# Kernel optimization log

Measured on AMD Instinct MI355X. Metric: run time of the kernel, lower is better.

Reference implementation:

```python
import jax, jax.numpy as jnp
import numpy as np

N, E, NIN, NOUT, H = 50000, 800000, 128, 128, 8
C = NOUT // H  # head dim = 16


def setup_inputs() -> dict:
    key = jax.random.key(0)
    ks = jax.random.split(key, 12)
    s = 1.0 / np.sqrt(NIN)
    return {
        "x": jax.random.normal(ks[0], (N, NIN), dtype=jnp.float32),
        "edge_index": jax.random.randint(ks[1], (2, E), 0, N),
        "edge_attr": jax.random.normal(ks[2], (E, NIN), dtype=jnp.float32),
        "Wq": jax.random.normal(ks[3], (NIN, H * C), dtype=jnp.float32) * s,
        "bq": jnp.zeros((H * C,), dtype=jnp.float32),
        "Wk": jax.random.normal(ks[4], (NIN, H * C), dtype=jnp.float32) * s,
        "bk": jnp.zeros((H * C,), dtype=jnp.float32),
        "Wv": jax.random.normal(ks[5], (NIN, H * C), dtype=jnp.float32) * s,
        "bv": jnp.zeros((H * C,), dtype=jnp.float32),
        "We": jax.random.normal(ks[6], (NIN, H * C), dtype=jnp.float32) * s,  # lin_edge, bias=False in PyG
        "Wskip": jax.random.normal(ks[7], (NIN, H * C), dtype=jnp.float32) * s,
        "bskip": jnp.zeros((H * C,), dtype=jnp.float32),
    }


def reference(x, edge_index, edge_attr, Wq, bq, Wk, bk, Wv, bv, We, Wskip, bskip):
    src = edge_index[0]  # j (source / message sender)
    dst = edge_index[1]  # i (destination / aggregation target)

    q = (x @ Wq + bq).reshape(N, H, C)
    k = (x @ Wk + bk).reshape(N, H, C)
    v = (x @ Wv + bv).reshape(N, H, C)
    e = (edge_attr @ We).reshape(E, H, C)

    k_e = k[src] + e                                   # [E,H,C]
    alpha = jnp.einsum('ehc,ehc->eh', q[dst], k_e) / jnp.sqrt(jnp.float32(C))

    # segment softmax over incoming edges of each destination node
    m = jax.ops.segment_max(alpha, dst, num_segments=N)            # [N,H]
    a = jnp.exp(alpha - m[dst])                                    # [E,H]
    z = jax.ops.segment_sum(a, dst, num_segments=N)                # [N,H]
    a = a / (z[dst] + 1e-16)

    msg = (v[src] + e) * a[:, :, None]                             # [E,H,C]
    out = jax.ops.segment_sum(msg, dst, num_segments=N)            # [N,H,C]
    out = out.reshape(N, H * C) + (x @ Wskip + bskip)              # root skip
    return out
```

## Files before the change

### kernel.cpp

```cpp
#include <hip/hip_runtime.h>


#define N_NODES 50000
#define N_EDGES 800000
#define DIN     128
#define DHC     128
#define NHEAD   8
#define HDIM    16
#define BK      32
#define LDAT    132

static_assert(N_EDGES % 128 == 0, "edge tiles exact");

__global__ __launch_bounds__(256) void node_gemm_kernel(
    const float* __restrict__ x,
    const float* __restrict__ Wq, const float* __restrict__ bq,
    const float* __restrict__ Wk, const float* __restrict__ bk,
    const float* __restrict__ Wv, const float* __restrict__ bv,
    const float* __restrict__ Wskip, const float* __restrict__ bskip,
    float* __restrict__ Q, float* __restrict__ K,
    float* __restrict__ V, float* __restrict__ SKIP)
{
    __shared__ float sXT[BK * LDAT];
    __shared__ float sW[BK * LDAT];

    const float* W; const float* bias; float* OUT;
    switch (blockIdx.y) {
        case 0:  W = Wq;    bias = bq;    OUT = Q;    break;
        case 1:  W = Wk;    bias = bk;    OUT = K;    break;
        case 2:  W = Wv;    bias = bv;    OUT = V;    break;
        default: W = Wskip; bias = bskip; OUT = SKIP; break;
    }

    const int tid  = threadIdx.x;
    const int row0 = blockIdx.x * 128;
    const int r0   = (tid >> 4) * 4;
    const int c0   = (tid & 15) * 4;

    float acc[8][8];
    #pragma unroll
    for (int i = 0; i < 8; ++i)
        #pragma unroll
        for (int j = 0; j < 8; ++j) acc[i][j] = 0.f;

    for (int kk = 0; kk < DIN; kk += BK) {
        #pragma unroll
        for (int p = 0; p < 4; ++p) {
            int i = tid + p * 256;
            int k = i >> 5, c4 = i & 31;
            ((float4*)&sW[k * LDAT])[c4] =
                ((const float4*)(W + (size_t)(kk + k) * DHC))[c4];
        }
        #pragma unroll
        for (int p = 0; p < 4; ++p) {
            int el = (tid >> 3) + p * 32;
            int c4 = tid & 7;
            int r  = row0 + el;
            float4 v = (r < N_NODES)
                ? ((const float4*)(x + (size_t)r * DIN + kk))[c4]
                : make_float4(0.f, 0.f, 0.f, 0.f);
            int kl = c4 * 4;
            sXT[(kl + 0) * LDAT + el] = v.x;
            sXT[(kl + 1) * LDAT + el] = v.y;
            sXT[(kl + 2) * LDAT + el] = v.z;
            sXT[(kl + 3) * LDAT + el] = v.w;
        }
        __syncthreads();

        #pragma unroll 4
        for (int k = 0; k < BK; ++k) {
            float4 a0 = *(const float4*)&sXT[k * LDAT + r0];
            float4 a1 = *(const float4*)&sXT[k * LDAT + r0 + 64];
            float4 b0 = *(const float4*)&sW[k * LDAT + c0];
            float4 b1 = *(const float4*)&sW[k * LDAT + c0 + 64];
            float a[8] = {a0.x, a0.y, a0.z, a0.w, a1.x, a1.y, a1.z, a1.w};
            float b[8] = {b0.x, b0.y, b0.z, b0.w, b1.x, b1.y, b1.z, b1.w};
            #pragma unroll
            for (int i = 0; i < 8; ++i)
                #pragma unroll
                for (int j = 0; j < 8; ++j)
                    acc[i][j] = fmaf(a[i], b[j], acc[i][j]);
        }
        __syncthreads();
    }

    float bcol[8];
    #pragma unroll
    for (int j = 0; j < 8; ++j) bcol[j] = bias[c0 + ((j < 4) ? j : j + 60)];

    #pragma unroll
    for (int i = 0; i < 8; ++i) {
        int r = row0 + r0 + ((i < 4) ? i : i + 60);
        if (r < N_NODES) {
            float4 o0 = make_float4(acc[i][0] + bcol[0], acc[i][1] + bcol[1],
                                    acc[i][2] + bcol[2], acc[i][3] + bcol[3]);
            float4 o1 = make_float4(acc[i][4] + bcol[4], acc[i][5] + bcol[5],
                                    acc[i][6] + bcol[6], acc[i][7] + bcol[7]);
            *(float4*)(OUT + (size_t)r * DHC + c0)      = o0;
            *(float4*)(OUT + (size_t)r * DHC + c0 + 64) = o1;
        }
    }
}

__global__ __launch_bounds__(256) void hist_kernel(
    const int* __restrict__ eidx, int* __restrict__ cnt)
{
    for (int i = blockIdx.x * 256 + threadIdx.x; i < N_EDGES; i += gridDim.x * 256)
        atomicAdd(&cnt[eidx[N_EDGES + i]], 1);
}

__global__ __launch_bounds__(1024) void scan_kernel(
    const int* __restrict__ cnt, int* __restrict__ cursor)
{
    __shared__ int buf[2][1024];
    const int tid = threadIdx.x;
    const int chunk = (N_NODES + 1023) / 1024;
    const int base = tid * chunk;
    int s = 0;
    for (int i = 0; i < chunk; ++i) {
        int idx = base + i;
        if (idx < N_NODES) s += cnt[idx];
    }
    buf[0][tid] = s;
    __syncthreads();
    int cur = 0;
    for (int off = 1; off < 1024; off <<= 1) {
        int v = buf[cur][tid];
        if (tid >= off) v += buf[cur][tid - off];
        buf[cur ^ 1][tid] = v;
        __syncthreads();
        cur ^= 1;
    }
    int run = buf[cur][tid] - s;
    for (int i = 0; i < chunk; ++i) {
        int idx = base + i;
        if (idx < N_NODES) {
            cursor[idx] = run;
            run += cnt[idx];
        }
    }
}

__global__ __launch_bounds__(256) void scatter_kernel(
    const int* __restrict__ eidx, int* __restrict__ cursor,
    int* __restrict__ s_eid, int* __restrict__ s_src, int* __restrict__ s_dst)
{
    for (int i = blockIdx.x * 256 + threadIdx.x; i < N_EDGES; i += gridDim.x * 256) {
        int d = eidx[N_EDGES + i];
        int pos = atomicAdd(&cursor[d], 1);
        s_eid[pos] = i;
        s_src[pos] = eidx[i];
        s_dst[pos] = d;
    }
}

__global__ __launch_bounds__(256) void edge_kernel(
    const float* __restrict__ edge_attr,
    const float* __restrict__ We,
    const int* __restrict__ s_eid, const int* __restrict__ s_src,
    const int* __restrict__ s_dst,
    const float* __restrict__ Qf, const float* __restrict__ Kf,
    const float* __restrict__ Vf,
    float* __restrict__ OUT,
    float* __restrict__ Z)
{
    __shared__ float pool[128 * LDAT];
    __shared__ float sw[128 * NHEAD];
    __shared__ int   sEid[128], sSrc[128], sDst[128];
    __shared__ unsigned long long smask[2];
    __shared__ int   runstart[130];

    float* sAT = pool;
    float* sB  = pool + BK * LDAT;

    const int tid = threadIdx.x;
    const int r0  = (tid >> 4) * 4;
    const int c0  = (tid & 15) * 4;
    const int nTiles = N_EDGES / 128;

    for (int tile = blockIdx.x; tile < nTiles; tile += gridDim.x) {
        const int e0 = tile * 128;
        __syncthreads();

        for (int i = tid; i < 3 * 128; i += 256) {
            int which = i >> 7, el = i & 127;
            if (which == 0)      sEid[el] = s_eid[e0 + el];
            else if (which == 1) sSrc[el] = s_src[e0 + el];
            else                 sDst[el] = s_dst[e0 + el];
        }
        __syncthreads();

        float acc[8][8];
        #pragma unroll
        for (int i = 0; i < 8; ++i)
            #pragma unroll
            for (int j = 0; j < 8; ++j) acc[i][j] = 0.f;

        for (int kk = 0; kk < DIN; kk += BK) {
            #pragma unroll
            for (int p = 0; p < 4; ++p) {
                int i = tid + p * 256;
                int k = i >> 5, c4 = i & 31;
                ((float4*)&sB[k * LDAT])[c4] =
                    ((const float4*)(We + (size_t)(kk + k) * DHC))[c4];
            }
            #pragma unroll
            for (int p = 0; p < 4; ++p) {
                int el = (tid >> 3) + p * 32;
                int c4 = tid & 7;
                float4 v = ((const float4*)(edge_attr + (size_t)sEid[el] * DIN + kk))[c4];
                int kl = c4 * 4;
                sAT[(kl + 0) * LDAT + el] = v.x;
                sAT[(kl + 1) * LDAT + el] = v.y;
                sAT[(kl + 2) * LDAT + el] = v.z;
                sAT[(kl + 3) * LDAT + el] = v.w;
            }
            __syncthreads();

            #pragma unroll 4
            for (int k = 0; k < BK; ++k) {
                float4 a0 = *(const float4*)&sAT[k * LDAT + r0];
                float4 a1 = *(const float4*)&sAT[k * LDAT + r0 + 64];
                float4 b0 = *(const float4*)&sB[k * LDAT + c0];
                float4 b1 = *(const float4*)&sB[k * LDAT + c0 + 64];
                float a[8] = {a0.x, a0.y, a0.z, a0.w, a1.x, a1.y, a1.z, a1.w};
                float b[8] = {b0.x, b0.y, b0.z, b0.w, b1.x, b1.y, b1.z, b1.w};
                #pragma unroll
                for (int i = 0; i < 8; ++i)
                    #pragma unroll
                    for (int j = 0; j < 8; ++j)
                        acc[i][j] = fmaf(a[i], b[j], acc[i][j]);
            }
            __syncthreads();
        }

        #pragma unroll
        for (int i = 0; i < 8; ++i) {
            int row = r0 + ((i < 4) ? i : i + 60);
            *(float4*)&pool[row * LDAT + c0] =
                make_float4(acc[i][0], acc[i][1], acc[i][2], acc[i][3]);
            *(float4*)&pool[row * LDAT + c0 + 64] =
                make_float4(acc[i][4], acc[i][5], acc[i][6], acc[i][7]);
        }
        __syncthreads();

        #pragma unroll
        for (int t = 0; t < 4; ++t) {
            int task = tid + t * 256;
            int el   = task & 127;
            int h    = task >> 7;
            int src  = sSrc[el];
            int dst  = sDst[el];
            const float4* qp = (const float4*)(Qf + (size_t)dst * DHC + h * HDIM);
            const float4* kp = (const float4*)(Kf + (size_t)src * DHC + h * HDIM);
            const float4* vp = (const float4*)(Vf + (size_t)src * DHC + h * HDIM);
            float4* ep = (float4*)&pool[el * LDAT + h * HDIM];

            float4 e4[4], q4[4], k4[4];
            #pragma unroll
            for (int r = 0; r < 4; ++r) { e4[r] = ep[r]; q4[r] = qp[r]; k4[r] = kp[r]; }

            float alpha = 0.f;
            #pragma unroll
            for (int r = 0; r < 4; ++r) {
                alpha = fmaf(q4[r].x, k4[r].x + e4[r].x, alpha);
                alpha = fmaf(q4[r].y, k4[r].y + e4[r].y, alpha);
                alpha = fmaf(q4[r].z, k4[r].z + e4[r].z, alpha);
                alpha = fmaf(q4[r].w, k4[r].w + e4[r].w, alpha);
            }
            float w = __expf(alpha * 0.25f);
            sw[el * NHEAD + h] = w;
            #pragma unroll
            for (int r = 0; r < 4; ++r) {
                float4 v4 = vp[r];
                ep[r] = make_float4(w * (v4.x + e4[r].x), w * (v4.y + e4[r].y),
                                    w * (v4.z + e4[r].z), w * (v4.w + e4[r].w));
            }
        }

        if (tid < 128) {
            bool flag = (tid == 0) || (sDst[tid] != sDst[tid - 1]);
            unsigned long long m = __ballot(flag);
            if ((tid & 63) == 0) smask[tid >> 6] = m;
        }
        __syncthreads();

        const unsigned long long m0 = smask[0], m1 = smask[1];
        const int nruns = __popcll(m0) + __popcll(m1);
        if (tid < 128) {
            bool flag = (tid == 0) || (sDst[tid] != sDst[tid - 1]);
            if (flag) {
                int rid;
                if (tid < 64) rid = __popcll(m0 & ((1ull << tid) - 1));
                else          rid = __popcll(m0) + __popcll(m1 & ((1ull << (tid - 64)) - 1));
                runstart[rid] = tid;
            }
        }
        if (tid == 0) runstart[nruns] = 128;
        __syncthreads();

        for (int t = tid; t < nruns * NHEAD; t += 256) {
            int r = t >> 3, h = t & 7;
            int s0 = runstart[r], s1 = runstart[r + 1];
            float s = 0.f;
            for (int el = s0; el < s1; ++el) s += sw[el * NHEAD + h];
            int dst = sDst[s0];
            if (r == 0 || r == nruns - 1) atomicAdd(&Z[(size_t)dst * NHEAD + h], s);
            else                          Z[(size_t)dst * NHEAD + h] = s;
        }

        for (int t = tid; t < nruns * 32; t += 256) {
            int r = t >> 5, c = t & 31;
            int s0 = runstart[r], s1 = runstart[r + 1];
            float4 s = make_float4(0.f, 0.f, 0.f, 0.f);
            for (int el = s0; el < s1; ++el) {
                float4 v = *(const float4*)&pool[el * LDAT + c * 4];
                s.x += v.x; s.y += v.y; s.z += v.z; s.w += v.w;
            }
            int dst = sDst[s0];
            float* ob = OUT + (size_t)dst * DHC + c * 4;
            if (r == 0 || r == nruns - 1) {
                atomicAdd(ob + 0, s.x); atomicAdd(ob + 1, s.y);
                atomicAdd(ob + 2, s.z); atomicAdd(ob + 3, s.w);
            } else {
                *(float4*)ob = s;
            }
        }
    }
}

__global__ __launch_bounds__(256) void finalize_kernel(
    float* __restrict__ OUT, const float* __restrict__ Z,
    const float* __restrict__ SKIP)
{
    size_t idx = (size_t)blockIdx.x * 256 + threadIdx.x;
    if (idx >= (size_t)N_NODES * DHC) return;
    int n = (int)(idx >> 7);
    int h = ((int)idx & 127) >> 4;
    OUT[idx] = OUT[idx] / (Z[(size_t)n * NHEAD + h] + 1e-16f) + SKIP[idx];
}

extern "C" void kernel_launch(void* const* d_in, const int* in_sizes, int n_in,
                              void* d_out, int out_size, void* d_ws, size_t ws_size,
                              hipStream_t stream)
{
    const float* x         = (const float*)d_in[0];
    const int*   eidx      = (const int*)  d_in[1];
    const float* edge_attr = (const float*)d_in[2];
    const float* Wq    = (const float*)d_in[3];
    const float* bq    = (const float*)d_in[4];
    const float* Wk    = (const float*)d_in[5];
    const float* bk    = (const float*)d_in[6];
    const float* Wv    = (const float*)d_in[7];
    const float* bv    = (const float*)d_in[8];
    const float* We    = (const float*)d_in[9];
    const float* Wskip = (const float*)d_in[10];
    const float* bskip = (const float*)d_in[11];
    float* out = (float*)d_out;

    float* ws = (float*)d_ws;
    const size_t npf = (size_t)N_NODES * DHC;
    float* Q      = ws;
    float* K      = ws + npf;
    float* V      = ws + 2 * npf;
    float* SKIP   = ws + 3 * npf;
    float* Z      = ws + 4 * npf;
    int*   cnt    = (int*)(ws + 4 * npf + (size_t)N_NODES * NHEAD);
    int*   cursor = cnt + N_NODES;
    int*   s_eid  = cursor + N_NODES;
    int*   s_src  = s_eid + N_EDGES;
    int*   s_dst  = s_src + N_EDGES;

    hipMemsetAsync(out, 0, npf * sizeof(float), stream);
    hipMemsetAsync(Z, 0, (size_t)N_NODES * NHEAD * sizeof(float), stream);
    hipMemsetAsync(cnt, 0, (size_t)N_NODES * sizeof(int), stream);

    dim3 gA((N_NODES + 127) / 128, 4);
    node_gemm_kernel<<<gA, 256, 0, stream>>>(x, Wq, bq, Wk, bk, Wv, bv, Wskip, bskip,
                                             Q, K, V, SKIP);

    hist_kernel<<<1024, 256, 0, stream>>>(eidx, cnt);
    scan_kernel<<<1, 1024, 0, stream>>>(cnt, cursor);
    scatter_kernel<<<1024, 256, 0, stream>>>(eidx, cursor, s_eid, s_src, s_dst);

    edge_kernel<<<1024, 256, 0, stream>>>(edge_attr, We, s_eid, s_src, s_dst,
                                          Q, K, V, out, Z);

    finalize_kernel<<<(int)((npf + 255) / 256), 256, 0, stream>>>(out, Z, SKIP);
}
```

Baseline: 1.188 ms.

## Use split-bf16 MFMA GEMMs for node and edge projections, pack edge metadata

Replaces the FP32 FMA tiled GEMMs in the node projection and edge projection kernels with bf16 MFMA 16x16x32 instructions. Operands are split into high and low bf16 parts and three MFMAs are used per tile to keep near-fp32 accuracy. A prep kernel pre-transposes and splits the weights. The three sorted edge arrays are packed into one int4 record so each edge tile needs a single coalesced load. The split adds conversion work and three times the MFMA count, plus scalar epilogue stores.

```diff
diff --git a/kernel.cpp b/kernel.cpp
--- a/kernel.cpp
+++ b/kernel.cpp
@@ -7,97 +7,149 @@
 #define DHC     128
 #define NHEAD   8
 #define HDIM    16
-#define BK      32
+#define LDK     72
 #define LDAT    132
 
 static_assert(N_EDGES % 128 == 0, "edge tiles exact");
 
-__global__ __launch_bounds__(256) void node_gemm_kernel(
+typedef short bf16x8 __attribute__((ext_vector_type(8)));
+typedef float f32x4  __attribute__((ext_vector_type(4)));
+
+#define MFMA(a, b, c) __builtin_amdgcn_mfma_f32_16x16x32_bf16((a), (b), (c), 0, 0, 0)
+
+__device__ __forceinline__ void split4(const float4 v, uint2& hi, uint2& lo) {
+    uint a0 = __float_as_uint(v.x), a1 = __float_as_uint(v.y);
+    uint a2 = __float_as_uint(v.z), a3 = __float_as_uint(v.w);
+    hi.x = (a1 & 0xFFFF0000u) | (a0 >> 16);
+    hi.y = (a3 & 0xFFFF0000u) | (a2 >> 16);
+    float d0 = v.x - __uint_as_float(a0 & 0xFFFF0000u);
+    float d1 = v.y - __uint_as_float(a1 & 0xFFFF0000u);
+    float d2 = v.z - __uint_as_float(a2 & 0xFFFF0000u);
+    float d3 = v.w - __uint_as_float(a3 & 0xFFFF0000u);
+    uint b0 = __float_as_uint(d0), b1 = __float_as_uint(d1);
+    uint b2 = __float_as_uint(d2), b3 = __float_as_uint(d3);
+    lo.x = (b1 & 0xFFFF0000u) | (b0 >> 16);
+    lo.y = (b3 & 0xFFFF0000u) | (b2 >> 16);
+}
+
+__global__ __launch_bounds__(256) void prep_weights(
+    const float* __restrict__ Wq, const float* __restrict__ Wk,
+    const float* __restrict__ Wv, const float* __restrict__ Wskip,
+    const float* __restrict__ We,
+    ushort* __restrict__ WTh, ushort* __restrict__ WTl)
+{
+    const float* W;
+    switch (blockIdx.y) {
+        case 0: W = Wq; break;  case 1: W = Wk; break;
+        case 2: W = Wv; break;  case 3: W = Wskip; break;
+        default: W = We; break;
+    }
+    ushort* th = WTh + (size_t)blockIdx.y * DIN * DHC;
+    ushort* tl = WTl + (size_t)blockIdx.y * DIN * DHC;
+
+    for (int i = blockIdx.x * 256 + threadIdx.x; i < DIN * 32; i += 1024) {
+        int k  = i >> 5;
+        int c4 = (i & 31) * 4;
+        float4 v = ((const float4*)(W + (size_t)k * DHC))[i & 31];
+        float e[4] = {v.x, v.y, v.z, v.w};
+        #pragma unroll
+        for (int j = 0; j < 4; ++j) {
+            uint a = __float_as_uint(e[j]);
+            th[(c4 + j) * DIN + k] = (ushort)(a >> 16);
+            float d = e[j] - __uint_as_float(a & 0xFFFF0000u);
+            tl[(c4 + j) * DIN + k] = (ushort)(__float_as_uint(d) >> 16);
+        }
+    }
+}
+
+__global__ __launch_bounds__(256) void node_gemm_mfma(
     const float* __restrict__ x,
-    const float* __restrict__ Wq, const float* __restrict__ bq,
-    const float* __restrict__ Wk, const float* __restrict__ bk,
-    const float* __restrict__ Wv, const float* __restrict__ bv,
-    const float* __restrict__ Wskip, const float* __restrict__ bskip,
+    const ushort* __restrict__ WTh, const ushort* __restrict__ WTl,
+    const float* __restrict__ bq, const float* __restrict__ bk,
+    const float* __restrict__ bv, const float* __restrict__ bskip,
     float* __restrict__ Q, float* __restrict__ K,
     float* __restrict__ V, float* __restrict__ SKIP)
 {
-    __shared__ float sXT[BK * LDAT];
-    __shared__ float sW[BK * LDAT];
-
-    const float* W; const float* bias; float* OUT;
-    switch (blockIdx.y) {
-        case 0:  W = Wq;    bias = bq;    OUT = Q;    break;
-        case 1:  W = Wk;    bias = bk;    OUT = K;    break;
-        case 2:  W = Wv;    bias = bv;    OUT = V;    break;
-        default: W = Wskip; bias = bskip; OUT = SKIP; break;
-    }
+    __shared__ ushort sAh[128 * LDK], sAl[128 * LDK];
+    __shared__ ushort sBh[128 * LDK], sBl[128 * LDK];
+
+    const int m = blockIdx.y;
+    const float* bias; float* OUT;
+    switch (m) {
+        case 0:  bias = bq;    OUT = Q;    break;
+        case 1:  bias = bk;    OUT = K;    break;
+        case 2:  bias = bv;    OUT = V;    break;
+        default: bias = bskip; OUT = SKIP; break;
+    }
+    const ushort* wh = WTh + (size_t)m * DIN * DHC;
+    const ushort* wl = WTl + (size_t)m * DIN * DHC;
 
     const int tid  = threadIdx.x;
     const int row0 = blockIdx.x * 128;
-    const int r0   = (tid >> 4) * 4;
-    const int c0   = (tid & 15) * 4;
-
-    float acc[8][8];
+    const int lane = tid & 63;
+    const int wv   = tid >> 6;
+    const int lr   = lane & 15;
+    const int lk   = lane >> 4;
+
+    f32x4 acc[8][2];
     #pragma unroll
-    for (int i = 0; i < 8; ++i)
-        #pragma unroll
-        for (int j = 0; j < 8; ++j) acc[i][j] = 0.f;
-
-    for (int kk = 0; kk < DIN; kk += BK) {
+    for (int i = 0; i < 8; ++i) { acc[i][0] = (f32x4)0.f; acc[i][1] = (f32x4)0.f; }
+
+    for (int kk = 0; kk < DIN; kk += 64) {
         #pragma unroll
         for (int p = 0; p < 4; ++p) {
             int i = tid + p * 256;
-            int k = i >> 5, c4 = i & 31;
-            ((float4*)&sW[k * LDAT])[c4] =
-                ((const float4*)(W + (size_t)(kk + k) * DHC))[c4];
-        }
-        #pragma unroll
-        for (int p = 0; p < 4; ++p) {
-            int el = (tid >> 3) + p * 32;
-            int c4 = tid & 7;
-            int r  = row0 + el;
+            int c = i >> 3, g = i & 7;
+            *(uint4*)&sBh[c * LDK + 8 * g] = *(const uint4*)(wh + c * DIN + kk + 8 * g);
+            *(uint4*)&sBl[c * LDK + 8 * g] = *(const uint4*)(wl + c * DIN + kk + 8 * g);
+        }
+        #pragma unroll
+        for (int p = 0; p < 8; ++p) {
+            int row = (tid >> 4) + 16 * p;
+            int c4  = tid & 15;
+            int r   = row0 + row;
             float4 v = (r < N_NODES)
                 ? ((const float4*)(x + (size_t)r * DIN + kk))[c4]
                 : make_float4(0.f, 0.f, 0.f, 0.f);
-            int kl = c4 * 4;
-            sXT[(kl + 0) * LDAT + el] = v.x;
-            sXT[(kl + 1) * LDAT + el] = v.y;
-            sXT[(kl + 2) * LDAT + el] = v.z;
-            sXT[(kl + 3) * LDAT + el] = v.w;
-        }
-        __syncthreads();
-
-        #pragma unroll 4
-        for (int k = 0; k < BK; ++k) {
-            float4 a0 = *(const float4*)&sXT[k * LDAT + r0];
-            float4 a1 = *(const float4*)&sXT[k * LDAT + r0 + 64];
-            float4 b0 = *(const float4*)&sW[k * LDAT + c0];
-            float4 b1 = *(const float4*)&sW[k * LDAT + c0 + 64];
-            float a[8] = {a0.x, a0.y, a0.z, a0.w, a1.x, a1.y, a1.z, a1.w};
-            float b[8] = {b0.x, b0.y, b0.z, b0.w, b1.x, b1.y, b1.z, b1.w};
-            #pragma unroll
-            for (int i = 0; i < 8; ++i)
-                #pragma unroll
-                for (int j = 0; j < 8; ++j)
-                    acc[i][j] = fmaf(a[i], b[j], acc[i][j]);
-        }
-        __syncthreads();
-    }
-
-    float bcol[8];
+            uint2 h, l; split4(v, h, l);
+            *(uint2*)&sAh[row * LDK + 4 * c4] = h;
+            *(uint2*)&sAl[row * LDK + 4 * c4] = l;
+        }
+        __syncthreads();
+
+        #pragma unroll
+        for (int ks = 0; ks < 2; ++ks) {
+            const int kb = ks * 32 + lk * 8;
+            bf16x8 bh0 = *(const bf16x8*)&sBh[(wv * 32 +      lr) * LDK + kb];
+            bf16x8 bh1 = *(const bf16x8*)&sBh[(wv * 32 + 16 + lr) * LDK + kb];
+            bf16x8 bl0 = *(const bf16x8*)&sBl[(wv * 32 +      lr) * LDK + kb];
+            bf16x8 bl1 = *(const bf16x8*)&sBl[(wv * 32 + 16 + lr) * LDK + kb];
+            #pragma unroll
+            for (int rf = 0; rf < 8; ++rf) {
+                bf16x8 ah = *(const bf16x8*)&sAh[(rf * 16 + lr) * LDK + kb];
+                bf16x8 al = *(const bf16x8*)&sAl[(rf * 16 + lr) * LDK + kb];
+                acc[rf][0] = MFMA(ah, bh0, acc[rf][0]);
+                acc[rf][0] = MFMA(al, bh0, acc[rf][0]);
+                acc[rf][0] = MFMA(ah, bl0, acc[rf][0]);
+                acc[rf][1] = MFMA(ah, bh1, acc[rf][1]);
+                acc[rf][1] = MFMA(al, bh1, acc[rf][1]);
+                acc[rf][1] = MFMA(ah, bl1, acc[rf][1]);
+            }
+        }
+        __syncthreads();
+    }
+
+    const float b0 = bias[wv * 32 + lr];
+    const float b1 = bias[wv * 32 + 16 + lr];
     #pragma unroll
-    for (int j = 0; j < 8; ++j) bcol[j] = bias[c0 + ((j < 4) ? j : j + 60)];
-
-    #pragma unroll
-    for (int i = 0; i < 8; ++i) {
-        int r = row0 + r0 + ((i < 4) ? i : i + 60);
-        if (r < N_NODES) {
-            float4 o0 = make_float4(acc[i][0] + bcol[0], acc[i][1] + bcol[1],
-                                    acc[i][2] + bcol[2], acc[i][3] + bcol[3]);
-            float4 o1 = make_float4(acc[i][4] + bcol[4], acc[i][5] + bcol[5],
-                                    acc[i][6] + bcol[6], acc[i][7] + bcol[7]);
-            *(float4*)(OUT + (size_t)r * DHC + c0)      = o0;
-            *(float4*)(OUT + (size_t)r * DHC + c0 + 64) = o1;
+    for (int rf = 0; rf < 8; ++rf) {
+        #pragma unroll
+        for (int reg = 0; reg < 4; ++reg) {
+            int r = row0 + rf * 16 + lk * 4 + reg;
+            if (r < N_NODES) {
+                OUT[(size_t)r * DHC + wv * 32 +      lr] = acc[rf][0][reg] + b0;
+                OUT[(size_t)r * DHC + wv * 32 + 16 + lr] = acc[rf][1][reg] + b1;
+            }
         }
     }
 }
@@ -143,104 +195,110 @@
 
 __global__ __launch_bounds__(256) void scatter_kernel(
     const int* __restrict__ eidx, int* __restrict__ cursor,
-    int* __restrict__ s_eid, int* __restrict__ s_src, int* __restrict__ s_dst)
+    int4* __restrict__ s_meta)
 {
     for (int i = blockIdx.x * 256 + threadIdx.x; i < N_EDGES; i += gridDim.x * 256) {
-        int d = eidx[N_EDGES + i];
+        int sv = eidx[i];
+        int d  = eidx[N_EDGES + i];
         int pos = atomicAdd(&cursor[d], 1);
-        s_eid[pos] = i;
-        s_src[pos] = eidx[i];
-        s_dst[pos] = d;
+        s_meta[pos] = make_int4(sv, d, i, 0);
     }
 }
 
 __global__ __launch_bounds__(256) void edge_kernel(
     const float* __restrict__ edge_attr,
-    const float* __restrict__ We,
-    const int* __restrict__ s_eid, const int* __restrict__ s_src,
-    const int* __restrict__ s_dst,
+    const ushort* __restrict__ WTh, const ushort* __restrict__ WTl,
+    const int4* __restrict__ s_meta,
     const float* __restrict__ Qf, const float* __restrict__ Kf,
     const float* __restrict__ Vf,
     float* __restrict__ OUT,
     float* __restrict__ Z)
 {
-    __shared__ float pool[128 * LDAT];
+    __shared__ __align__(16) char poolraw[4 * 128 * LDK * 2];
     __shared__ float sw[128 * NHEAD];
-    __shared__ int   sEid[128], sSrc[128], sDst[128];
+    __shared__ int   sSrc[128], sDst[128], sEid[128];
     __shared__ unsigned long long smask[2];
     __shared__ int   runstart[130];
 
-    float* sAT = pool;
-    float* sB  = pool + BK * LDAT;
-
-    const int tid = threadIdx.x;
-    const int r0  = (tid >> 4) * 4;
-    const int c0  = (tid & 15) * 4;
+    ushort* sAh = (ushort*)poolraw;
+    ushort* sAl = sAh + 128 * LDK;
+    ushort* sBh = sAl + 128 * LDK;
+    ushort* sBl = sBh + 128 * LDK;
+    float*  ep  = (float*)poolraw;
+
+    const ushort* wh = WTh + 4 * DIN * DHC;
+    const ushort* wl = WTl + 4 * DIN * DHC;
+
+    const int tid  = threadIdx.x;
+    const int lane = tid & 63;
+    const int wv   = tid >> 6;
+    const int lr   = lane & 15;
+    const int lk   = lane >> 4;
     const int nTiles = N_EDGES / 128;
 
     for (int tile = blockIdx.x; tile < nTiles; tile += gridDim.x) {
         const int e0 = tile * 128;
         __syncthreads();
 
-        for (int i = tid; i < 3 * 128; i += 256) {
-            int which = i >> 7, el = i & 127;
-            if (which == 0)      sEid[el] = s_eid[e0 + el];
-            else if (which == 1) sSrc[el] = s_src[e0 + el];
-            else                 sDst[el] = s_dst[e0 + el];
-        }
-        __syncthreads();
-
-        float acc[8][8];
-        #pragma unroll
-        for (int i = 0; i < 8; ++i)
-            #pragma unroll
-            for (int j = 0; j < 8; ++j) acc[i][j] = 0.f;
-
-        for (int kk = 0; kk < DIN; kk += BK) {
+        if (tid < 128) {
+            int4 mm = s_meta[e0 + tid];
+            sSrc[tid] = mm.x; sDst[tid] = mm.y; sEid[tid] = mm.z;
+        }
+        __syncthreads();
+
+        f32x4 acc[8][2];
+        #pragma unroll
+        for (int i = 0; i < 8; ++i) { acc[i][0] = (f32x4)0.f; acc[i][1] = (f32x4)0.f; }
+
+        for (int kk = 0; kk < DIN; kk += 64) {
             #pragma unroll
             for (int p = 0; p < 4; ++p) {
                 int i = tid + p * 256;
-                int k = i >> 5, c4 = i & 31;
-                ((float4*)&sB[k * LDAT])[c4] =
-                    ((const float4*)(We + (size_t)(kk + k) * DHC))[c4];
-            }
-            #pragma unroll
-            for (int p = 0; p < 4; ++p) {
-                int el = (tid >> 3) + p * 32;
-                int c4 = tid & 7;
-                float4 v = ((const float4*)(edge_attr + (size_t)sEid[el] * DIN + kk))[c4];
-                int kl = c4 * 4;
-                sAT[(kl + 0) * LDAT + el] = v.x;
-                sAT[(kl + 1) * LDAT + el] = v.y;
-                sAT[(kl + 2) * LDAT + el] = v.z;
-                sAT[(kl + 3) * LDAT + el] = v.w;
+                int c = i >> 3, g = i & 7;
+                *(uint4*)&sBh[c * LDK + 8 * g] = *(const uint4*)(wh + c * DIN + kk + 8 * g);
+                *(uint4*)&sBl[c * LDK + 8 * g] = *(const uint4*)(wl + c * DIN + kk + 8 * g);
+            }
+            #pragma unroll
+            for (int p = 0; p < 8; ++p) {
+                int row = (tid >> 4) + 16 * p;
+                int c4  = tid & 15;
+                float4 v = ((const float4*)(edge_attr + (size_t)sEid[row] * DIN + kk))[c4];
+                uint2 h, l; split4(v, h, l);
+                *(uint2*)&sAh[row * LDK + 4 * c4] = h;
+                *(uint2*)&sAl[row * LDK + 4 * c4] = l;
             }
             __syncthreads();
 
-            #pragma unroll 4
-            for (int k = 0; k < BK; ++k) {
-                float4 a0 = *(const float4*)&sAT[k * LDAT + r0];
-                float4 a1 = *(const float4*)&sAT[k * LDAT + r0 + 64];
-                float4 b0 = *(const float4*)&sB[k * LDAT + c0];
-                float4 b1 = *(const float4*)&sB[k * LDAT + c0 + 64];
-                float a[8] = {a0.x, a0.y, a0.z, a0.w, a1.x, a1.y, a1.z, a1.w};
-                float b[8] = {b0.x, b0.y, b0.z, b0.w, b1.x, b1.y, b1.z, b1.w};
+            #pragma unroll
+            for (int ks = 0; ks < 2; ++ks) {
+                const int kb = ks * 32 + lk * 8;
+                bf16x8 bh0 = *(const bf16x8*)&sBh[(wv * 32 +      lr) * LDK + kb];
+                bf16x8 bh1 = *(const bf16x8*)&sBh[(wv * 32 + 16 + lr) * LDK + kb];
+                bf16x8 bl0 = *(const bf16x8*)&sBl[(wv * 32 +      lr) * LDK + kb];
+                bf16x8 bl1 = *(const bf16x8*)&sBl[(wv * 32 + 16 + lr) * LDK + kb];
                 #pragma unroll
-                for (int i = 0; i < 8; ++i)
-                    #pragma unroll
-                    for (int j = 0; j < 8; ++j)
-                        acc[i][j] = fmaf(a[i], b[j], acc[i][j]);
+                for (int rf = 0; rf < 8; ++rf) {
+                    bf16x8 ah = *(const bf16x8*)&sAh[(rf * 16 + lr) * LDK + kb];
+                    bf16x8 al = *(const bf16x8*)&sAl[(rf * 16 + lr) * LDK + kb];
+                    acc[rf][0] = MFMA(ah, bh0, acc[rf][0]);
+                    acc[rf][0] = MFMA(al, bh0, acc[rf][0]);
+                    acc[rf][0] = MFMA(ah, bl0, acc[rf][0]);
+                    acc[rf][1] = MFMA(ah, bh1, acc[rf][1]);
+                    acc[rf][1] = MFMA(al, bh1, acc[rf][1]);
+                    acc[rf][1] = MFMA(ah, bl1, acc[rf][1]);
+                }
             }
             __syncthreads();
         }
 
         #pragma unroll
-        for (int i = 0; i < 8; ++i) {
-            int row = r0 + ((i < 4) ? i : i + 60);
-            *(float4*)&pool[row * LDAT + c0] =
-                make_float4(acc[i][0], acc[i][1], acc[i][2], acc[i][3]);
-            *(float4*)&pool[row * LDAT + c0 + 64] =
-                make_float4(acc[i][4], acc[i][5], acc[i][6], acc[i][7]);
+        for (int rf = 0; rf < 8; ++rf) {
+            #pragma unroll
+            for (int reg = 0; reg < 4; ++reg) {
+                int row = rf * 16 + lk * 4 + reg;
+                ep[row * LDAT + wv * 32 +      lr] = acc[rf][0][reg];
+                ep[row * LDAT + wv * 32 + 16 + lr] = acc[rf][1][reg];
+            }
         }
         __syncthreads();
 
@@ -254,11 +312,11 @@
             const float4* qp = (const float4*)(Qf + (size_t)dst * DHC + h * HDIM);
             const float4* kp = (const float4*)(Kf + (size_t)src * DHC + h * HDIM);
             const float4* vp = (const float4*)(Vf + (size_t)src * DHC + h * HDIM);
-            float4* ep = (float4*)&pool[el * LDAT + h * HDIM];
+            float4* epp = (float4*)&ep[el * LDAT + h * HDIM];
 
             float4 e4[4], q4[4], k4[4];
             #pragma unroll
-            for (int r = 0; r < 4; ++r) { e4[r] = ep[r]; q4[r] = qp[r]; k4[r] = kp[r]; }
+            for (int r = 0; r < 4; ++r) { e4[r] = epp[r]; q4[r] = qp[r]; k4[r] = kp[r]; }
 
             float alpha = 0.f;
             #pragma unroll
@@ -273,8 +331,8 @@
             #pragma unroll
             for (int r = 0; r < 4; ++r) {
                 float4 v4 = vp[r];
-                ep[r] = make_float4(w * (v4.x + e4[r].x), w * (v4.y + e4[r].y),
-                                    w * (v4.z + e4[r].z), w * (v4.w + e4[r].w));
+                epp[r] = make_float4(w * (v4.x + e4[r].x), w * (v4.y + e4[r].y),
+                                     w * (v4.z + e4[r].z), w * (v4.w + e4[r].w));
             }
         }
 
@@ -314,7 +372,7 @@
             int s0 = runstart[r], s1 = runstart[r + 1];
             float4 s = make_float4(0.f, 0.f, 0.f, 0.f);
             for (int el = s0; el < s1; ++el) {
-                float4 v = *(const float4*)&pool[el * LDAT + c * 4];
+                float4 v = *(const float4*)&ep[el * LDAT + c * 4];
                 s.x += v.x; s.y += v.y; s.z += v.z; s.w += v.w;
             }
             int dst = sDst[s0];
@@ -358,32 +416,33 @@
     const float* bskip = (const float*)d_in[11];
     float* out = (float*)d_out;
 
-    float* ws = (float*)d_ws;
+    char* wsb = (char*)d_ws;
     const size_t npf = (size_t)N_NODES * DHC;
-    float* Q      = ws;
-    float* K      = ws + npf;
-    float* V      = ws + 2 * npf;
-    float* SKIP   = ws + 3 * npf;
-    float* Z      = ws + 4 * npf;
-    int*   cnt    = (int*)(ws + 4 * npf + (size_t)N_NODES * NHEAD);
-    int*   cursor = cnt + N_NODES;
-    int*   s_eid  = cursor + N_NODES;
-    int*   s_src  = s_eid + N_EDGES;
-    int*   s_dst  = s_src + N_EDGES;
+    float* Q      = (float*)wsb;                          wsb += npf * 4;
+    float* K      = (float*)wsb;                          wsb += npf * 4;
+    float* V      = (float*)wsb;                          wsb += npf * 4;
+    float* SKIP   = (float*)wsb;                          wsb += npf * 4;
+    float* Z      = (float*)wsb;                          wsb += (size_t)N_NODES * NHEAD * 4;
+    int*   cnt    = (int*)wsb;                            wsb += (size_t)N_NODES * 4;
+    int*   cursor = (int*)wsb;                            wsb += (size_t)N_NODES * 4;
+    int4*  s_meta = (int4*)wsb;                           wsb += (size_t)N_EDGES * 16;
+    ushort* WTh   = (ushort*)wsb;                         wsb += (size_t)5 * DIN * DHC * 2;
+    ushort* WTl   = (ushort*)wsb;
 
     hipMemsetAsync(out, 0, npf * sizeof(float), stream);
     hipMemsetAsync(Z, 0, (size_t)N_NODES * NHEAD * sizeof(float), stream);
     hipMemsetAsync(cnt, 0, (size_t)N_NODES * sizeof(int), stream);
 
-    dim3 gA((N_NODES + 127) / 128, 4);
-    node_gemm_kernel<<<gA, 256, 0, stream>>>(x, Wq, bq, Wk, bk, Wv, bv, Wskip, bskip,
-                                             Q, K, V, SKIP);
+    prep_weights<<<dim3(4, 5), 256, 0, stream>>>(Wq, Wk, Wv, Wskip, We, WTh, WTl);
+
+    node_gemm_mfma<<<dim3((N_NODES + 127) / 128, 4), 256, 0, stream>>>(
+        x, WTh, WTl, bq, bk, bv, bskip, Q, K, V, SKIP);
 
     hist_kernel<<<1024, 256, 0, stream>>>(eidx, cnt);
     scan_kernel<<<1, 1024, 0, stream>>>(cnt, cursor);
-    scatter_kernel<<<1024, 256, 0, stream>>>(eidx, cursor, s_eid, s_src, s_dst);
-
-    edge_kernel<<<1024, 256, 0, stream>>>(edge_attr, We, s_eid, s_src, s_dst,
+    scatter_kernel<<<1024, 256, 0, stream>>>(eidx, cursor, s_meta);
+
+    edge_kernel<<<1024, 256, 0, stream>>>(edge_attr, WTh, WTl, s_meta,
                                           Q, K, V, out, Z);
 
     finalize_kernel<<<(int)((npf + 255) / 256), 256, 0, stream>>>(out, Z, SKIP);
```

Measured after the change: 1.101 ms. 1.08x faster.
